# Performance work log

Hardware: AMD Instinct MI355X
Metric: run time of the kernel (lower is better)

Reference implementation:

```python
import math
import jax, jax.numpy as jnp
import numpy as np

CAPACITY_FACTOR = 1.0
MIN_CAPACITY = 8


def setup_inputs() -> dict:
    key = jax.random.key(0)
    k1, k2 = jax.random.split(key)
    s, d, e = 8192, 1024, 64
    inputs = jax.random.normal(k1, (s, d), dtype=jnp.float32)
    wg_weight = jax.random.normal(k2, (e, d), dtype=jnp.float32) * (1.0 / math.sqrt(d))
    return {"inputs": inputs, "wg_weight": wg_weight}


def reference(inputs, wg_weight):
    # gate projection (always fp32 in the original)
    logits = inputs.astype(jnp.float32) @ wg_weight.T  # [s, e]
    s, e = logits.shape
    # static capacity: ceil(s/e * capacity_factor), floored at min_capacity
    capacity = max(int(math.ceil(s / e * CAPACITY_FACTOR)), MIN_CAPACITY)

    gates = jax.nn.softmax(logits, axis=1)            # [s, e]
    indices = jnp.argmax(gates, axis=1)               # [s]
    mask = jax.nn.one_hot(indices, e, dtype=jnp.int32)  # [s, e]
    exp_counts = jnp.sum(mask, axis=0)                # [e]

    # load-balancing aux loss (uses mask BEFORE capacity dropping)
    me = jnp.mean(gates, axis=0)
    ce = jnp.mean(mask.astype(jnp.float32), axis=0)
    l_aux = jnp.sum(me * ce) * e

    # capacity dropping: with use_rts=False, topk over the binary mask keeps
    # the first `capacity` tokens routed to each expert, i.e. cumulative
    # position-in-expert < capacity
    positions = jnp.cumsum(mask, axis=0) - 1          # [s, e]
    mask = mask * (positions < capacity).astype(jnp.int32)

    locations = jnp.cumsum(mask, axis=0) - 1          # [s, e]
    locations_s = jnp.sum(locations * mask, axis=1)   # [s] slot per token

    gates = gates * mask.astype(jnp.float32)          # zero out dropped tokens
    locations_sc = jax.nn.one_hot(locations_s, capacity, dtype=jnp.float32)  # [s, c]
    combine_weights = jnp.einsum('se,sc->sec', gates, locations_sc)  # [s, e, c]
    dispatch_mask = combine_weights.astype(bool)
    return l_aux, combine_weights, dispatch_mask, exp_counts
```

## Files before the change

### kernel.cpp

```cpp
#include <hip/hip_runtime.h>
#include <cstdint>
#include <cstddef>

#define S 8192
#define Dm 1024
#define E 64
#define CAP 128
#define SEC 67108864ull

#define GEMM_BLOCKS 256
#define FILL_BLOCKS 1792
#define N4ALL 33554448u
#define WSCALE 4096.0f
#define INV_WSCALE (1.0f / 4096.0f)

typedef float f32x4 __attribute__((ext_vector_type(4)));
typedef _Float16 f16x8 __attribute__((ext_vector_type(8)));
typedef float f32x4b __attribute__((ext_vector_type(4)));

#define CV8(H, L, ROW, COL, V0, V1, SCALE) do {                                \
    f16x8 hh, ll; float t_;                                                    \
    t_ = (V0).x * (SCALE); hh[0] = (_Float16)t_; ll[0] = (_Float16)(t_ - (float)hh[0]); \
    t_ = (V0).y * (SCALE); hh[1] = (_Float16)t_; ll[1] = (_Float16)(t_ - (float)hh[1]); \
    t_ = (V0).z * (SCALE); hh[2] = (_Float16)t_; ll[2] = (_Float16)(t_ - (float)hh[2]); \
    t_ = (V0).w * (SCALE); hh[3] = (_Float16)t_; ll[3] = (_Float16)(t_ - (float)hh[3]); \
    t_ = (V1).x * (SCALE); hh[4] = (_Float16)t_; ll[4] = (_Float16)(t_ - (float)hh[4]); \
    t_ = (V1).y * (SCALE); hh[5] = (_Float16)t_; ll[5] = (_Float16)(t_ - (float)hh[5]); \
    t_ = (V1).z * (SCALE); hh[6] = (_Float16)t_; ll[6] = (_Float16)(t_ - (float)hh[6]); \
    t_ = (V1).w * (SCALE); hh[7] = (_Float16)t_; ll[7] = (_Float16)(t_ - (float)hh[7]); \
    *(f16x8*)&H[ROW][COL] = hh;                                                \
    *(f16x8*)&L[ROW][COL] = ll;                                                \
} while (0)

__global__ __launch_bounds__(256) void k_main(const float* __restrict__ x,
                                              const float* __restrict__ w,
                                              float* __restrict__ gate,
                                              int* __restrict__ idx,
                                              float* __restrict__ me_part,
                                              float* __restrict__ out) {
    int bid = blockIdx.x;
    int tid = threadIdx.x;
    if (bid < GEMM_BLOCKS) {
        __shared__ _Float16 Ah[32][80];
        __shared__ _Float16 Alo[32][80];
        __shared__ _Float16 Wh[64][80];
        __shared__ _Float16 Wlo[64][80];
        __shared__ float Sl[32][66];
        __shared__ float sm[32];
        __shared__ float sinv[32];
        int t0 = bid * 32;
        int sr = tid >> 3;
        int sc = (tid & 7) * 8;
        const float* asrc = x + (size_t)(t0 + sr) * Dm + (tid & 7) * 8;
        const float* wsrc0 = w + (size_t)sr * Dm + (tid & 7) * 8;
        const float* wsrc1 = wsrc0 + 32 * (size_t)Dm;

        int wv = tid >> 6;
        int l = tid & 63;
        int lr = l & 15;
        int lg = l >> 4;
        int mt = wv & 1;
        int np = wv >> 1;
        f32x4b acc0 = {0.f, 0.f, 0.f, 0.f};
        f32x4b acc1 = {0.f, 0.f, 0.f, 0.f};

        float4 pa0 = *(const float4*)(asrc + 0);
        float4 pa1 = *(const float4*)(asrc + 4);
        float4 pw0 = *(const float4*)(wsrc0 + 0);
        float4 pw1 = *(const float4*)(wsrc0 + 4);
        float4 pw2 = *(const float4*)(wsrc1 + 0);
        float4 pw3 = *(const float4*)(wsrc1 + 4);
        float4 qa0 = *(const float4*)(asrc + 64);
        float4 qa1 = *(const float4*)(asrc + 68);
        float4 qw0 = *(const float4*)(wsrc0 + 64);
        float4 qw1 = *(const float4*)(wsrc0 + 68);
        float4 qw2 = *(const float4*)(wsrc1 + 64);
        float4 qw3 = *(const float4*)(wsrc1 + 68);

#define WRITE_LDS(A0, A1, W0, W1, W2, W3)                                      \
        CV8(Ah, Alo, sr, sc, A0, A1, 1.0f);                                    \
        CV8(Wh, Wlo, sr, sc, W0, W1, WSCALE);                                  \
        CV8(Wh, Wlo, (32 + sr), sc, W2, W3, WSCALE);

#define LOADP(KB)                                                              \
        pa0 = *(const float4*)(asrc + (KB));                                   \
        pa1 = *(const float4*)(asrc + (KB) + 4);                               \
        pw0 = *(const float4*)(wsrc0 + (KB));                                  \
        pw1 = *(const float4*)(wsrc0 + (KB) + 4);                              \
        pw2 = *(const float4*)(wsrc1 + (KB));                                  \
        pw3 = *(const float4*)(wsrc1 + (KB) + 4);

#define LOADQ(KB)                                                              \
        qa0 = *(const float4*)(asrc + (KB));                                   \
        qa1 = *(const float4*)(asrc + (KB) + 4);                               \
        qw0 = *(const float4*)(wsrc0 + (KB));                                  \
        qw1 = *(const float4*)(wsrc0 + (KB) + 4);                              \
        qw2 = *(const float4*)(wsrc1 + (KB));                                  \
        qw3 = *(const float4*)(wsrc1 + (KB) + 4);

#define INNER_MFMA                                                             \
        _Pragma("unroll")                                                      \
        for (int ks = 0; ks < 2; ++ks) {                                       \
            int kc = ks * 32 + lg * 8;                                         \
            f16x8 ah = *(const f16x8*)&Ah[mt * 16 + lr][kc];                   \
            f16x8 al = *(const f16x8*)&Alo[mt * 16 + lr][kc];                  \
            f16x8 bh0 = *(const f16x8*)&Wh[np * 32 + lr][kc];                  \
            f16x8 bl0 = *(const f16x8*)&Wlo[np * 32 + lr][kc];                 \
            f16x8 bh1 = *(const f16x8*)&Wh[np * 32 + 16 + lr][kc];             \
            f16x8 bl1 = *(const f16x8*)&Wlo[np * 32 + 16 + lr][kc];            \
            acc0 = __builtin_amdgcn_mfma_f32_16x16x32_f16(ah, bh0, acc0, 0, 0, 0); \
            acc0 = __builtin_amdgcn_mfma_f32_16x16x32_f16(al, bh0, acc0, 0, 0, 0); \
            acc0 = __builtin_amdgcn_mfma_f32_16x16x32_f16(ah, bl0, acc0, 0, 0, 0); \
            acc1 = __builtin_amdgcn_mfma_f32_16x16x32_f16(ah, bh1, acc1, 0, 0, 0); \
            acc1 = __builtin_amdgcn_mfma_f32_16x16x32_f16(al, bh1, acc1, 0, 0, 0); \
            acc1 = __builtin_amdgcn_mfma_f32_16x16x32_f16(ah, bl1, acc1, 0, 0, 0); \
        }

        for (int ch = 0; ch < 16; ch += 2) {
            __syncthreads();
            WRITE_LDS(pa0, pa1, pw0, pw1, pw2, pw3)
            __syncthreads();
            if (ch + 2 < 16) { LOADP((ch + 2) * 64) }
            INNER_MFMA
            __syncthreads();
            WRITE_LDS(qa0, qa1, qw0, qw1, qw2, qw3)
            __syncthreads();
            if (ch + 3 < 16) { LOADQ((ch + 3) * 64) }
            INNER_MFMA
        }
#undef WRITE_LDS
#undef LOADP
#undef LOADQ
#undef INNER_MFMA
        __syncthreads();
#pragma unroll
        for (int r = 0; r < 4; ++r) {
            Sl[mt * 16 + lg * 4 + r][np * 32 + lr] = acc0[r] * INV_WSCALE;
            Sl[mt * 16 + lg * 4 + r][np * 32 + 16 + lr] = acc1[r] * INV_WSCALE;
        }
        __syncthreads();
        if (tid < 32) {
            float m = Sl[tid][0];
            int am = 0;
#pragma unroll
            for (int c = 1; c < E; ++c) {
                float v = Sl[tid][c];
                if (v > m) { m = v; am = c; }
            }
            float ssum = 0.f;
#pragma unroll
            for (int c = 0; c < E; ++c) ssum += __expf(Sl[tid][c] - m);
            float inv = 1.0f / ssum;
            gate[t0 + tid] = inv;
            idx[t0 + tid] = am;
            sm[tid] = m;
            sinv[tid] = inv;
        }
        __syncthreads();
        if (tid < E) {
            float cs = 0.f;
#pragma unroll 8
            for (int r = 0; r < 32; ++r)
                cs += __expf(Sl[r][tid] - sm[r]) * sinv[r];
            me_part[bid * E + tid] = cs;
        }
    } else {
        int fb = bid - GEMM_BLOCKS;
        f32x4 z = {0.f, 0.f, 0.f, 0.f};
        f32x4* o4 = (f32x4*)out;
        for (unsigned i = (unsigned)fb * 256u + tid; i < N4ALL;
             i += FILL_BLOCKS * 256u)
            o4[i] = z;
    }
}

__global__ __launch_bounds__(256) void k_scan(const int* __restrict__ idx,
                                              const float* __restrict__ gate,
                                              const float* __restrict__ me_part,
                                              float* __restrict__ out) {
    int e = blockIdx.x;
    int tid = threadIdx.x;
    int lane = tid & 63;
    int wid = tid >> 6;
    __shared__ int wsum[4];
    __shared__ float red[256];
    int running = 0;
    for (int ch = 0; ch < S / 256; ++ch) {
        int t = ch * 256 + tid;
        bool f = (idx[t] == e);
        unsigned long long b = __ballot(f);
        int pre = __popcll(b & ((1ull << lane) - 1ull));
        if (lane == 0) wsum[wid] = __popcll(b);
        __syncthreads();
        int off = running;
#pragma unroll
        for (int w2 = 0; w2 < 4; ++w2)
            if (w2 < wid) off += wsum[w2];
        int p = off + pre;
        if (f && p < CAP) {
            size_t o = 1 + (size_t)t * (E * CAP) + (size_t)e * CAP + (size_t)p;
            out[o] = gate[t];
            out[o + (size_t)SEC] = 1.0f;
        }
        running += wsum[0] + wsum[1] + wsum[2] + wsum[3];
        __syncthreads();
    }
    red[tid] = me_part[tid * E + e];
    __syncthreads();
    for (int s2 = 128; s2 > 0; s2 >>= 1) {
        if (tid < s2) red[tid] += red[tid + s2];
        __syncthreads();
    }
    if (tid == 0) {
        out[1 + 2 * (size_t)SEC + e] = (float)running;
        float la = red[0] * (1.0f / (float)S) *
                   ((float)running / (float)S) * (float)E;
        atomicAdd(out, la);
    }
}

extern "C" void kernel_launch(void* const* d_in, const int* in_sizes, int n_in,
                              void* d_out, int out_size, void* d_ws, size_t ws_size,
                              hipStream_t stream) {
    const float* x = (const float*)d_in[0];
    const float* w = (const float*)d_in[1];
    float* out = (float*)d_out;

    float* me_part = (float*)d_ws;
    float* gate = me_part + GEMM_BLOCKS * E;
    int* idx = (int*)(gate + S);

    k_main<<<dim3(GEMM_BLOCKS + FILL_BLOCKS), dim3(256), 0, stream>>>(
        x, w, gate, idx, me_part, out);
    k_scan<<<dim3(64), dim3(256), 0, stream>>>(idx, gate, me_part, out);
}
```

Before: 136.7 us.

## Enlarge gate GEMM tile to 128 tokens per 512-thread block

Raises each GEMM block from 32 to 128 tokens with 8 waves, each wave covering all 64 experts, so the weight tile loaded into LDS is shared across more tokens. The GEMM block count drops from 256 to 64 and the fill blocks are reorganised to 960 blocks of 512 threads. Shared memory grows to about 56KB per block, with the logits scratch buffer aliasing the operand buffers. The aim is less redundant weight traffic and conversion work, at the cost of fewer, heavier GEMM blocks and lower occupancy while the large zero-fill runs alongside.

```diff
diff --git a/kernel.cpp b/kernel.cpp
--- a/kernel.cpp
+++ b/kernel.cpp
@@ -8,31 +8,28 @@
 #define CAP 128
 #define SEC 67108864ull
 
-#define GEMM_BLOCKS 256
-#define FILL_BLOCKS 1792
+#define GEMM_BLOCKS 64
+#define FILL_BLOCKS 960
+#define NTHR 512
 #define N4ALL 33554448u
 #define WSCALE 4096.0f
 #define INV_WSCALE (1.0f / 4096.0f)
 
 typedef float f32x4 __attribute__((ext_vector_type(4)));
+typedef _Float16 f16x4 __attribute__((ext_vector_type(4)));
 typedef _Float16 f16x8 __attribute__((ext_vector_type(8)));
-typedef float f32x4b __attribute__((ext_vector_type(4)));
-
-#define CV8(H, L, ROW, COL, V0, V1, SCALE) do {                                \
-    f16x8 hh, ll; float t_;                                                    \
-    t_ = (V0).x * (SCALE); hh[0] = (_Float16)t_; ll[0] = (_Float16)(t_ - (float)hh[0]); \
-    t_ = (V0).y * (SCALE); hh[1] = (_Float16)t_; ll[1] = (_Float16)(t_ - (float)hh[1]); \
-    t_ = (V0).z * (SCALE); hh[2] = (_Float16)t_; ll[2] = (_Float16)(t_ - (float)hh[2]); \
-    t_ = (V0).w * (SCALE); hh[3] = (_Float16)t_; ll[3] = (_Float16)(t_ - (float)hh[3]); \
-    t_ = (V1).x * (SCALE); hh[4] = (_Float16)t_; ll[4] = (_Float16)(t_ - (float)hh[4]); \
-    t_ = (V1).y * (SCALE); hh[5] = (_Float16)t_; ll[5] = (_Float16)(t_ - (float)hh[5]); \
-    t_ = (V1).z * (SCALE); hh[6] = (_Float16)t_; ll[6] = (_Float16)(t_ - (float)hh[6]); \
-    t_ = (V1).w * (SCALE); hh[7] = (_Float16)t_; ll[7] = (_Float16)(t_ - (float)hh[7]); \
-    *(f16x8*)&H[ROW][COL] = hh;                                                \
-    *(f16x8*)&L[ROW][COL] = ll;                                                \
+
+#define CV4(H, L, ROW, COL, V, SCALE) do {                                     \
+    f16x4 hh, ll; float t_;                                                    \
+    t_ = (V).x * (SCALE); hh[0] = (_Float16)t_; ll[0] = (_Float16)(t_ - (float)hh[0]); \
+    t_ = (V).y * (SCALE); hh[1] = (_Float16)t_; ll[1] = (_Float16)(t_ - (float)hh[1]); \
+    t_ = (V).z * (SCALE); hh[2] = (_Float16)t_; ll[2] = (_Float16)(t_ - (float)hh[2]); \
+    t_ = (V).w * (SCALE); hh[3] = (_Float16)t_; ll[3] = (_Float16)(t_ - (float)hh[3]); \
+    *(f16x4*)&H[ROW][COL] = hh;                                                \
+    *(f16x4*)&L[ROW][COL] = ll;                                                \
 } while (0)
 
-__global__ __launch_bounds__(256) void k_main(const float* __restrict__ x,
+__global__ __launch_bounds__(512) void k_main(const float* __restrict__ x,
                                               const float* __restrict__ w,
                                               float* __restrict__ gate,
                                               int* __restrict__ idx,
@@ -41,105 +38,110 @@
     int bid = blockIdx.x;
     int tid = threadIdx.x;
     if (bid < GEMM_BLOCKS) {
-        __shared__ _Float16 Ah[32][80];
-        __shared__ _Float16 Alo[32][80];
-        __shared__ _Float16 Wh[64][80];
-        __shared__ _Float16 Wlo[64][80];
-        __shared__ float Sl[32][66];
-        __shared__ float sm[32];
-        __shared__ float sinv[32];
-        int t0 = bid * 32;
-        int sr = tid >> 3;
-        int sc = (tid & 7) * 8;
-        const float* asrc = x + (size_t)(t0 + sr) * Dm + (tid & 7) * 8;
-        const float* wsrc0 = w + (size_t)sr * Dm + (tid & 7) * 8;
-        const float* wsrc1 = wsrc0 + 32 * (size_t)Dm;
+        __shared__ __align__(16) char smem[56320];
+        _Float16 (*Ah)[72]  = (_Float16(*)[72])(smem);
+        _Float16 (*Alo)[72] = (_Float16(*)[72])(smem + 18432);
+        _Float16 (*Wh)[72]  = (_Float16(*)[72])(smem + 36864);
+        _Float16 (*Wlo)[72] = (_Float16(*)[72])(smem + 46080);
+        float (*Sl)[66] = (float(*)[66])(smem);
+        float* sm = (float*)(smem + 55296);
+        float* sinv = (float*)(smem + 55808);
+        int t0 = bid * 128;
+        int ar = tid >> 4;
+        int ac = (tid & 15) * 4;
+        int wr = tid >> 3;
+        int wc = (tid & 7) * 8;
+        const float* asrc = x + (size_t)(t0 + ar) * Dm + ac;
+        const float* wsrc = w + (size_t)wr * Dm + wc;
 
         int wv = tid >> 6;
         int l = tid & 63;
         int lr = l & 15;
         int lg = l >> 4;
-        int mt = wv & 1;
-        int np = wv >> 1;
-        f32x4b acc0 = {0.f, 0.f, 0.f, 0.f};
-        f32x4b acc1 = {0.f, 0.f, 0.f, 0.f};
-
-        float4 pa0 = *(const float4*)(asrc + 0);
-        float4 pa1 = *(const float4*)(asrc + 4);
-        float4 pw0 = *(const float4*)(wsrc0 + 0);
-        float4 pw1 = *(const float4*)(wsrc0 + 4);
-        float4 pw2 = *(const float4*)(wsrc1 + 0);
-        float4 pw3 = *(const float4*)(wsrc1 + 4);
-        float4 qa0 = *(const float4*)(asrc + 64);
-        float4 qa1 = *(const float4*)(asrc + 68);
-        float4 qw0 = *(const float4*)(wsrc0 + 64);
-        float4 qw1 = *(const float4*)(wsrc0 + 68);
-        float4 qw2 = *(const float4*)(wsrc1 + 64);
-        float4 qw3 = *(const float4*)(wsrc1 + 68);
-
-#define WRITE_LDS(A0, A1, W0, W1, W2, W3)                                      \
-        CV8(Ah, Alo, sr, sc, A0, A1, 1.0f);                                    \
-        CV8(Wh, Wlo, sr, sc, W0, W1, WSCALE);                                  \
-        CV8(Wh, Wlo, (32 + sr), sc, W2, W3, WSCALE);
-
+        f32x4 acc0 = {0.f, 0.f, 0.f, 0.f};
+        f32x4 acc1 = {0.f, 0.f, 0.f, 0.f};
+        f32x4 acc2 = {0.f, 0.f, 0.f, 0.f};
+        f32x4 acc3 = {0.f, 0.f, 0.f, 0.f};
+
+        float4 pa0, pa1, pa2, pa3, pw0, pw1;
+        float4 qa0, qa1, qa2, qa3, qw0, qw1;
 #define LOADP(KB)                                                              \
         pa0 = *(const float4*)(asrc + (KB));                                   \
-        pa1 = *(const float4*)(asrc + (KB) + 4);                               \
-        pw0 = *(const float4*)(wsrc0 + (KB));                                  \
-        pw1 = *(const float4*)(wsrc0 + (KB) + 4);                              \
-        pw2 = *(const float4*)(wsrc1 + (KB));                                  \
-        pw3 = *(const float4*)(wsrc1 + (KB) + 4);
-
+        pa1 = *(const float4*)(asrc + 32 * Dm + (KB));                         \
+        pa2 = *(const float4*)(asrc + 64 * Dm + (KB));                         \
+        pa3 = *(const float4*)(asrc + 96 * Dm + (KB));                         \
+        pw0 = *(const float4*)(wsrc + (KB));                                   \
+        pw1 = *(const float4*)(wsrc + (KB) + 4);
 #define LOADQ(KB)                                                              \
         qa0 = *(const float4*)(asrc + (KB));                                   \
-        qa1 = *(const float4*)(asrc + (KB) + 4);                               \
-        qw0 = *(const float4*)(wsrc0 + (KB));                                  \
-        qw1 = *(const float4*)(wsrc0 + (KB) + 4);                              \
-        qw2 = *(const float4*)(wsrc1 + (KB));                                  \
-        qw3 = *(const float4*)(wsrc1 + (KB) + 4);
-
+        qa1 = *(const float4*)(asrc + 32 * Dm + (KB));                         \
+        qa2 = *(const float4*)(asrc + 64 * Dm + (KB));                         \
+        qa3 = *(const float4*)(asrc + 96 * Dm + (KB));                         \
+        qw0 = *(const float4*)(wsrc + (KB));                                   \
+        qw1 = *(const float4*)(wsrc + (KB) + 4);
+#define WRITE_LDS(A0, A1, A2, A3, W0, W1)                                      \
+        CV4(Ah, Alo, ar, ac, A0, 1.0f);                                        \
+        CV4(Ah, Alo, (ar + 32), ac, A1, 1.0f);                                 \
+        CV4(Ah, Alo, (ar + 64), ac, A2, 1.0f);                                 \
+        CV4(Ah, Alo, (ar + 96), ac, A3, 1.0f);                                 \
+        CV4(Wh, Wlo, wr, wc, W0, WSCALE);                                      \
+        CV4(Wh, Wlo, wr, (wc + 4), W1, WSCALE);
 #define INNER_MFMA                                                             \
         _Pragma("unroll")                                                      \
         for (int ks = 0; ks < 2; ++ks) {                                       \
             int kc = ks * 32 + lg * 8;                                         \
-            f16x8 ah = *(const f16x8*)&Ah[mt * 16 + lr][kc];                   \
-            f16x8 al = *(const f16x8*)&Alo[mt * 16 + lr][kc];                  \
-            f16x8 bh0 = *(const f16x8*)&Wh[np * 32 + lr][kc];                  \
-            f16x8 bl0 = *(const f16x8*)&Wlo[np * 32 + lr][kc];                 \
-            f16x8 bh1 = *(const f16x8*)&Wh[np * 32 + 16 + lr][kc];             \
-            f16x8 bl1 = *(const f16x8*)&Wlo[np * 32 + 16 + lr][kc];            \
+            f16x8 ah = *(const f16x8*)&Ah[wv * 16 + lr][kc];                   \
+            f16x8 al = *(const f16x8*)&Alo[wv * 16 + lr][kc];                  \
+            f16x8 bh0 = *(const f16x8*)&Wh[lr][kc];                            \
+            f16x8 bl0 = *(const f16x8*)&Wlo[lr][kc];                           \
+            f16x8 bh1 = *(const f16x8*)&Wh[16 + lr][kc];                       \
+            f16x8 bl1 = *(const f16x8*)&Wlo[16 + lr][kc];                      \
+            f16x8 bh2 = *(const f16x8*)&Wh[32 + lr][kc];                       \
+            f16x8 bl2 = *(const f16x8*)&Wlo[32 + lr][kc];                      \
+            f16x8 bh3 = *(const f16x8*)&Wh[48 + lr][kc];                       \
+            f16x8 bl3 = *(const f16x8*)&Wlo[48 + lr][kc];                      \
             acc0 = __builtin_amdgcn_mfma_f32_16x16x32_f16(ah, bh0, acc0, 0, 0, 0); \
             acc0 = __builtin_amdgcn_mfma_f32_16x16x32_f16(al, bh0, acc0, 0, 0, 0); \
             acc0 = __builtin_amdgcn_mfma_f32_16x16x32_f16(ah, bl0, acc0, 0, 0, 0); \
             acc1 = __builtin_amdgcn_mfma_f32_16x16x32_f16(ah, bh1, acc1, 0, 0, 0); \
             acc1 = __builtin_amdgcn_mfma_f32_16x16x32_f16(al, bh1, acc1, 0, 0, 0); \
             acc1 = __builtin_amdgcn_mfma_f32_16x16x32_f16(ah, bl1, acc1, 0, 0, 0); \
-        }
-
+            acc2 = __builtin_amdgcn_mfma_f32_16x16x32_f16(ah, bh2, acc2, 0, 0, 0); \
+            acc2 = __builtin_amdgcn_mfma_f32_16x16x32_f16(al, bh2, acc2, 0, 0, 0); \
+            acc2 = __builtin_amdgcn_mfma_f32_16x16x32_f16(ah, bl2, acc2, 0, 0, 0); \
+            acc3 = __builtin_amdgcn_mfma_f32_16x16x32_f16(ah, bh3, acc3, 0, 0, 0); \
+            acc3 = __builtin_amdgcn_mfma_f32_16x16x32_f16(al, bh3, acc3, 0, 0, 0); \
+            acc3 = __builtin_amdgcn_mfma_f32_16x16x32_f16(ah, bl3, acc3, 0, 0, 0); \
+        }
+
+        LOADP(0)
+        LOADQ(64)
         for (int ch = 0; ch < 16; ch += 2) {
             __syncthreads();
-            WRITE_LDS(pa0, pa1, pw0, pw1, pw2, pw3)
+            WRITE_LDS(pa0, pa1, pa2, pa3, pw0, pw1)
             __syncthreads();
             if (ch + 2 < 16) { LOADP((ch + 2) * 64) }
             INNER_MFMA
             __syncthreads();
-            WRITE_LDS(qa0, qa1, qw0, qw1, qw2, qw3)
+            WRITE_LDS(qa0, qa1, qa2, qa3, qw0, qw1)
             __syncthreads();
             if (ch + 3 < 16) { LOADQ((ch + 3) * 64) }
             INNER_MFMA
         }
-#undef WRITE_LDS
 #undef LOADP
 #undef LOADQ
+#undef WRITE_LDS
 #undef INNER_MFMA
         __syncthreads();
 #pragma unroll
         for (int r = 0; r < 4; ++r) {
-            Sl[mt * 16 + lg * 4 + r][np * 32 + lr] = acc0[r] * INV_WSCALE;
-            Sl[mt * 16 + lg * 4 + r][np * 32 + 16 + lr] = acc1[r] * INV_WSCALE;
-        }
-        __syncthreads();
-        if (tid < 32) {
+            Sl[wv * 16 + lg * 4 + r][lr] = acc0[r] * INV_WSCALE;
+            Sl[wv * 16 + lg * 4 + r][16 + lr] = acc1[r] * INV_WSCALE;
+            Sl[wv * 16 + lg * 4 + r][32 + lr] = acc2[r] * INV_WSCALE;
+            Sl[wv * 16 + lg * 4 + r][48 + lr] = acc3[r] * INV_WSCALE;
+        }
+        __syncthreads();
+        if (tid < 128) {
             float m = Sl[tid][0];
             int am = 0;
 #pragma unroll
@@ -160,7 +162,7 @@
         if (tid < E) {
             float cs = 0.f;
 #pragma unroll 8
-            for (int r = 0; r < 32; ++r)
+            for (int r = 0; r < 128; ++r)
                 cs += __expf(Sl[r][tid] - sm[r]) * sinv[r];
             me_part[bid * E + tid] = cs;
         }
@@ -168,8 +170,8 @@
         int fb = bid - GEMM_BLOCKS;
         f32x4 z = {0.f, 0.f, 0.f, 0.f};
         f32x4* o4 = (f32x4*)out;
-        for (unsigned i = (unsigned)fb * 256u + tid; i < N4ALL;
-             i += FILL_BLOCKS * 256u)
+        for (unsigned i = (unsigned)fb * NTHR + tid; i < N4ALL;
+             i += FILL_BLOCKS * NTHR)
             o4[i] = z;
     }
 }
@@ -205,7 +207,7 @@
         running += wsum[0] + wsum[1] + wsum[2] + wsum[3];
         __syncthreads();
     }
-    red[tid] = me_part[tid * E + e];
+    red[tid] = (tid < GEMM_BLOCKS) ? me_part[tid * E + e] : 0.f;
     __syncthreads();
     for (int s2 = 128; s2 > 0; s2 >>= 1) {
         if (tid < s2) red[tid] += red[tid + s2];
@@ -230,7 +232,7 @@
     float* gate = me_part + GEMM_BLOCKS * E;
     int* idx = (int*)(gate + S);
 
-    k_main<<<dim3(GEMM_BLOCKS + FILL_BLOCKS), dim3(256), 0, stream>>>(
+    k_main<<<dim3(GEMM_BLOCKS + FILL_BLOCKS), dim3(NTHR), 0, stream>>>(
         x, w, gate, idx, me_part, out);
     k_scan<<<dim3(64), dim3(256), 0, stream>>>(idx, gate, me_part, out);
 }
```

Measured after the change: 143.7 us. +5.2%, slower.
